# Kernel optimization log

Hardware: AMD Instinct MI355X
Metric: run time of the kernel (lower is better)

The kernel has to match this reference:

```python
import jax, jax.numpy as jnp
import numpy as np

N = 10000      # num nodes
E = 320000     # num edges
IN = 256       # in_dim
MP = 256       # mp_width
FL = 512       # fl_width
OUT = 64       # out_dim


def setup_inputs() -> dict:
    key = jax.random.key(0)
    ks = jax.random.split(key, 20)
    inp = {}
    inp["x"] = jax.random.normal(ks[0], (N, IN), dtype=jnp.float32)
    inp["edge_index"] = jax.random.randint(ks[1], (2, E), 0, N, dtype=jnp.int64)
    # iMP (frozen) linear layers: weight ~ N(0, 1) per nn.init.normal_(std=1.0)
    inp["mp_w0"] = jax.random.normal(ks[2], (IN, MP), dtype=jnp.float32)
    inp["mp_b0"] = jax.random.uniform(ks[3], (MP,), minval=-1.0, maxval=1.0) / np.sqrt(IN)
    inp["mp_w1"] = jax.random.normal(ks[4], (MP, MP), dtype=jnp.float32)
    inp["mp_b1"] = jax.random.uniform(ks[5], (MP,), minval=-1.0, maxval=1.0) / np.sqrt(MP)
    inp["mp_w2"] = jax.random.normal(ks[6], (MP, MP), dtype=jnp.float32)
    inp["mp_b2"] = jax.random.uniform(ks[7], (MP,), minval=-1.0, maxval=1.0) / np.sqrt(MP)
    # FC layers (torch default Linear init scale ~ 1/sqrt(fan_in))
    inp["fc_w0"] = jax.random.normal(ks[8], (MP, FL), dtype=jnp.float32) / np.sqrt(MP)
    inp["fc_b0"] = jnp.zeros((FL,), dtype=jnp.float32)
    inp["fc_w1"] = jax.random.normal(ks[9], (FL, FL), dtype=jnp.float32) / np.sqrt(FL)
    inp["fc_b1"] = jnp.zeros((FL,), dtype=jnp.float32)
    # injection projections
    inp["inj_w0"] = jax.random.normal(ks[10], (MP, FL), dtype=jnp.float32) / np.sqrt(MP)
    inp["inj_b0"] = jnp.zeros((FL,), dtype=jnp.float32)
    inp["inj_w1"] = jax.random.normal(ks[11], (MP, FL), dtype=jnp.float32) / np.sqrt(MP)
    inp["inj_b1"] = jnp.zeros((FL,), dtype=jnp.float32)
    inp["alpha"] = jnp.array(1.0, dtype=jnp.float32)
    inp["out_w"] = jax.random.normal(ks[12], (FL, OUT), dtype=jnp.float32) / np.sqrt(FL)
    inp["out_b"] = jnp.zeros((OUT,), dtype=jnp.float32)
    return inp


def _imp(x, w, b, row, col, deg_inv):
    # h = relu(W x); h /= deg; Ah = scatter_add over row of h[col]
    h = jax.nn.relu(x @ w + b) * deg_inv[:, None]      # [N, out]
    return jnp.zeros_like(h).at[row].add(h[col])       # gather + scatter-add


def reference(x, edge_index, mp_w0, mp_b0, mp_w1, mp_b1, mp_w2, mp_b2,
              fc_w0, fc_b0, fc_w1, fc_b1, inj_w0, inj_b0, inj_w1, inj_b1,
              alpha, out_w, out_b):
    row, col = edge_index[0], edge_index[1]
    deg = jax.ops.segment_sum(jnp.ones((E,), x.dtype), col, num_segments=N)
    # nodes with deg==0 never appear in col so clamping does not change output
    deg_inv = 1.0 / jnp.maximum(deg, 1.0)

    h = _imp(x, mp_w0, mp_b0, row, col, deg_inv)
    h = _imp(h, mp_w1, mp_b1, row, col, deg_inv)
    h = _imp(h, mp_w2, mp_b2, row, col, deg_inv)

    x_inject = h
    h = alpha * (jax.nn.relu(h) @ fc_w0 + fc_b0) + (x_inject @ inj_w0 + inj_b0)
    h = alpha * (jax.nn.relu(h) @ fc_w1 + fc_b1) + (x_inject @ inj_w1 + inj_b1)
    return h @ out_w + out_b
```

## Files before the change

kernel.cpp:

```cpp
#include <hip/hip_runtime.h>

#define N_NODES 10000
#define N_EDGES 320000
#define MPAD 10112
#define NBIN 10048
#define CAP 128
#define ECHUNK 1024
#define EBLKS 313
#define PREP_BLOCKS 1735
#define PREP_TOT 1148480L

typedef unsigned short u16;
typedef short bf16x8 __attribute__((ext_vector_type(8)));
typedef float f32x4 __attribute__((ext_vector_type(4)));

__device__ __forceinline__ u16 f2b(float f) {
  unsigned u = __builtin_bit_cast(unsigned, f);
  unsigned r = u + 0x7fffu + ((u >> 16) & 1u);
  return (u16)(r >> 16);
}
__device__ __forceinline__ unsigned pack2(float a, float b) {
  return (unsigned)f2b(a) | ((unsigned)f2b(b) << 16);
}
__device__ __forceinline__ float blo(unsigned u) { return __builtin_bit_cast(float, u << 16); }
__device__ __forceinline__ float bhi(unsigned u) { return __builtin_bit_cast(float, u & 0xffff0000u); }

struct PP {
  const float *x; const int *ei;
  const float *w0, *w1, *w2, *fcw0, *injw0, *fcw1, *injw1, *outw;
  const float *fcb0, *injb0, *fcb1, *injb1, *alpha, *outb;
  u16 *xb, *w0t, *w1t, *w2t, *wc1t, *wft;
  float *bias1, *bf;
  int *cursor, *deg, *csr;
};

__global__ __launch_bounds__(256) void prep_place(PP P) {
  const int tid = threadIdx.x, bid = blockIdx.x;

  if (bid < EBLKS) {
    const int e0 = bid * ECHUNK;
#pragma unroll
    for (int j = 0; j < ECHUNK; j += 256) {
      int e = e0 + j + tid;
      if (e < N_EDGES) {
        int r = P.ei[e];
        int c = P.ei[N_EDGES + e];
        int pos = atomicAdd(&P.cursor[r], 1);
        if (pos < CAP) P.csr[r * CAP + pos] = c;
        atomicAdd(&P.deg[c], 1);
      }
    }
    return;
  }

  const float alpha = P.alpha[0];
  const long stride = (long)PREP_BLOCKS * 256;
  for (long ii = (long)(bid - EBLKS) * 256 + tid; ii < PREP_TOT; ii += stride) {
    long i = ii;
    if (i < 640000L) {
      float4 v = ((const float4*)P.x)[i];
      uint2 o;
      o.x = pack2(v.x, v.y);
      o.y = pack2(v.z, v.w);
      *(uint2*)(P.xb + 4 * i) = o;
      continue;
    }
    i -= 640000L;
    if (i < 65536) { P.w0t[i] = f2b(P.w0[(i & 255) * 256 + (i >> 8)]); continue; }
    i -= 65536;
    if (i < 65536) { P.w1t[i] = f2b(P.w1[(i & 255) * 256 + (i >> 8)]); continue; }
    i -= 65536;
    if (i < 65536) { P.w2t[i] = f2b(P.w2[(i & 255) * 256 + (i >> 8)]); continue; }
    i -= 65536;
    if (i < 262144) {
      int n = (int)(i >> 9), k = (int)(i & 511);
      float v = (k < 256) ? alpha * P.fcw0[k * 512 + n] : P.injw0[(k - 256) * 512 + n];
      P.wc1t[i] = f2b(v); continue;
    }
    i -= 262144;
    if (i < 49152) {
      int n = (int)(i & 63), k = (int)(i >> 6);
      const float* fr = (k < 512) ? P.fcw1 + (size_t)k * 512
                                  : P.injw1 + (size_t)(k - 512) * 512;
      float a0 = 0.f, a1 = 0.f, a2 = 0.f, a3 = 0.f;
#pragma unroll 4
      for (int j = 0; j < 512; j += 4) {
        float4 f = *(const float4*)(fr + j);
        a0 += f.x * P.outw[(j + 0) * 64 + n];
        a1 += f.y * P.outw[(j + 1) * 64 + n];
        a2 += f.z * P.outw[(j + 2) * 64 + n];
        a3 += f.w * P.outw[(j + 3) * 64 + n];
      }
      float acc = (a0 + a1) + (a2 + a3);
      if (k < 512) acc *= alpha;
      P.wft[n * 768 + k] = f2b(acc);
      continue;
    }
    i -= 49152;
    if (i < 64) {
      float acc = P.outb[i];
#pragma unroll 8
      for (int j = 0; j < 512; ++j)
        acc += (alpha * P.fcb1[j] + P.injb1[j]) * P.outw[j * 64 + i];
      P.bf[i] = acc;
      continue;
    }
    i -= 64;
    if (i < 512) { P.bias1[i] = alpha * P.fcb0[i] + P.injb0[i]; continue; }
  }
}

template<int K, bool RELU, bool SCALE, bool F32OUT>
__global__ __launch_bounds__(128) void gemm64(
    const u16* __restrict__ A, int lda,
    const u16* __restrict__ Bt,
    const float* __restrict__ bias,
    const int* __restrict__ deg,
    u16* __restrict__ Cb, float* __restrict__ Cf, int ldc)
{
  __shared__ u16 As[64 * 72];
  __shared__ u16 Bs[64 * 72];
  const int tid = threadIdx.x;
  const int m0 = blockIdx.x * 64;
  const int n0 = blockIdx.y * 64;
  const int wave = tid >> 6;
  const int lane = tid & 63;
  const int wr = wave * 32;
  const int lm = lane & 15;
  const int koff = (lane >> 4) * 8;

  const int srow = tid >> 2;
  const int scol = (tid & 3) * 16;
  const u16* Ag0 = A + (size_t)(m0 + srow) * lda + scol;
  const u16* Ag1 = A + (size_t)(m0 + srow + 32) * lda + scol;
  const u16* Bg0 = Bt + (size_t)(n0 + srow) * K + scol;
  const u16* Bg1 = Bt + (size_t)(n0 + srow + 32) * K + scol;
  u16* Asw0 = &As[srow * 72 + scol];
  u16* Asw1 = &As[(srow + 32) * 72 + scol];
  u16* Bsw0 = &Bs[srow * 72 + scol];
  u16* Bsw1 = &Bs[(srow + 32) * 72 + scol];

  f32x4 acc[2][4] = {};

  int4 pa0 = *(const int4*)(Ag0),     pa1 = *(const int4*)(Ag0 + 8);
  int4 pa2 = *(const int4*)(Ag1),     pa3 = *(const int4*)(Ag1 + 8);
  int4 pb0 = *(const int4*)(Bg0),     pb1 = *(const int4*)(Bg0 + 8);
  int4 pb2 = *(const int4*)(Bg1),     pb3 = *(const int4*)(Bg1 + 8);

#pragma unroll
  for (int kb = 0; kb < K; kb += 64) {
    __syncthreads();
    *(int4*)Asw0 = pa0; *(int4*)(Asw0 + 8) = pa1;
    *(int4*)Asw1 = pa2; *(int4*)(Asw1 + 8) = pa3;
    *(int4*)Bsw0 = pb0; *(int4*)(Bsw0 + 8) = pb1;
    *(int4*)Bsw1 = pb2; *(int4*)(Bsw1 + 8) = pb3;
    __syncthreads();
    if (kb + 64 < K) {
      pa0 = *(const int4*)(Ag0 + kb + 64); pa1 = *(const int4*)(Ag0 + kb + 72);
      pa2 = *(const int4*)(Ag1 + kb + 64); pa3 = *(const int4*)(Ag1 + kb + 72);
      pb0 = *(const int4*)(Bg0 + kb + 64); pb1 = *(const int4*)(Bg0 + kb + 72);
      pb2 = *(const int4*)(Bg1 + kb + 64); pb3 = *(const int4*)(Bg1 + kb + 72);
    }
#pragma unroll
    for (int ks = 0; ks < 2; ++ks) {
      bf16x8 af[2], bf[4];
#pragma unroll
      for (int mi = 0; mi < 2; ++mi)
        af[mi] = *(const bf16x8*)&As[(wr + mi * 16 + lm) * 72 + ks * 32 + koff];
#pragma unroll
      for (int ni = 0; ni < 4; ++ni)
        bf[ni] = *(const bf16x8*)&Bs[(ni * 16 + lm) * 72 + ks * 32 + koff];
#pragma unroll
      for (int mi = 0; mi < 2; ++mi)
#pragma unroll
        for (int ni = 0; ni < 4; ++ni)
          acc[mi][ni] = __builtin_amdgcn_mfma_f32_16x16x32_bf16(af[mi], bf[ni], acc[mi][ni], 0, 0, 0);
    }
  }

  const int q4 = (lane >> 4) * 4;
#pragma unroll
  for (int mi = 0; mi < 2; ++mi) {
#pragma unroll
    for (int ni = 0; ni < 4; ++ni) {
      const int gc = n0 + ni * 16 + lm;
      const float bv = bias[gc];
#pragma unroll
      for (int r = 0; r < 4; ++r) {
        const int gr = m0 + wr + mi * 16 + q4 + r;
        float v = acc[mi][ni][r] + bv;
        if (RELU) v = fmaxf(v, 0.f);
        if (SCALE) v *= 1.0f / fmaxf((float)deg[gr], 1.0f);
        if (F32OUT) {
          if (gr < N_NODES) Cf[(size_t)gr * ldc + gc] = v;
        } else {
          Cb[(size_t)gr * ldc + gc] = f2b(v);
        }
      }
    }
  }
}

__global__ __launch_bounds__(128) void gemm_fold(
    const u16* __restrict__ Ar,
    const u16* __restrict__ Ah,
    const u16* __restrict__ Bt,
    const float* __restrict__ bias,
    float* __restrict__ Cf)
{
  const int K = 768;
  __shared__ u16 As[64 * 72];
  __shared__ u16 Bs[64 * 72];
  const int tid = threadIdx.x;
  const int m0 = blockIdx.x * 64;
  const int wave = tid >> 6;
  const int lane = tid & 63;
  const int wr = wave * 32;
  const int lm = lane & 15;
  const int koff = (lane >> 4) * 8;

  const int srow = tid >> 2;
  const int scol = (tid & 3) * 16;
  const int ar0 = m0 + srow, ar1 = m0 + srow + 32;
  auto aptr = [&](int row, int col) -> const u16* {
    return (col < 512) ? Ar + (size_t)row * 512 + col
                       : Ah + (size_t)row * 512 + (col - 512);
  };
  const u16* Bg0 = Bt + (size_t)srow * K + scol;
  const u16* Bg1 = Bt + (size_t)(srow + 32) * K + scol;
  u16* Asw0 = &As[srow * 72 + scol];
  u16* Asw1 = &As[(srow + 32) * 72 + scol];
  u16* Bsw0 = &Bs[srow * 72 + scol];
  u16* Bsw1 = &Bs[(srow + 32) * 72 + scol];

  f32x4 acc[2][4] = {};

  int4 pa0 = *(const int4*)aptr(ar0, scol);
  int4 pa1 = *(const int4*)aptr(ar0, scol + 8);
  int4 pa2 = *(const int4*)aptr(ar1, scol);
  int4 pa3 = *(const int4*)aptr(ar1, scol + 8);
  int4 pb0 = *(const int4*)(Bg0), pb1 = *(const int4*)(Bg0 + 8);
  int4 pb2 = *(const int4*)(Bg1), pb3 = *(const int4*)(Bg1 + 8);

#pragma unroll
  for (int kb = 0; kb < K; kb += 64) {
    __syncthreads();
    *(int4*)Asw0 = pa0; *(int4*)(Asw0 + 8) = pa1;
    *(int4*)Asw1 = pa2; *(int4*)(Asw1 + 8) = pa3;
    *(int4*)Bsw0 = pb0; *(int4*)(Bsw0 + 8) = pb1;
    *(int4*)Bsw1 = pb2; *(int4*)(Bsw1 + 8) = pb3;
    __syncthreads();
    if (kb + 64 < K) {
      int c = kb + 64 + scol;
      pa0 = *(const int4*)aptr(ar0, c);
      pa1 = *(const int4*)aptr(ar0, c + 8);
      pa2 = *(const int4*)aptr(ar1, c);
      pa3 = *(const int4*)aptr(ar1, c + 8);
      pb0 = *(const int4*)(Bg0 + kb + 64); pb1 = *(const int4*)(Bg0 + kb + 72);
      pb2 = *(const int4*)(Bg1 + kb + 64); pb3 = *(const int4*)(Bg1 + kb + 72);
    }
#pragma unroll
    for (int ks = 0; ks < 2; ++ks) {
      bf16x8 af[2], bf[4];
#pragma unroll
      for (int mi = 0; mi < 2; ++mi)
        af[mi] = *(const bf16x8*)&As[(wr + mi * 16 + lm) * 72 + ks * 32 + koff];
#pragma unroll
      for (int ni = 0; ni < 4; ++ni)
        bf[ni] = *(const bf16x8*)&Bs[(ni * 16 + lm) * 72 + ks * 32 + koff];
#pragma unroll
      for (int mi = 0; mi < 2; ++mi)
#pragma unroll
        for (int ni = 0; ni < 4; ++ni)
          acc[mi][ni] = __builtin_amdgcn_mfma_f32_16x16x32_bf16(af[mi], bf[ni], acc[mi][ni], 0, 0, 0);
    }
  }

  const int q4 = (lane >> 4) * 4;
#pragma unroll
  for (int mi = 0; mi < 2; ++mi) {
#pragma unroll
    for (int ni = 0; ni < 4; ++ni) {
      const int gc = ni * 16 + lm;
      const float bv = bias[gc];
#pragma unroll
      for (int r = 0; r < 4; ++r) {
        const int gr = m0 + wr + mi * 16 + q4 + r;
        if (gr < N_NODES) Cf[(size_t)gr * 64 + gc] = acc[mi][ni][r] + bv;
      }
    }
  }
}

__global__ __launch_bounds__(256) void aggregate(
    const u16* __restrict__ tmp, const int* __restrict__ cnt,
    const int* __restrict__ csr, u16* __restrict__ out0,
    u16* __restrict__ A1, int mode)
{
  const int wv = threadIdx.x >> 6;
  const int lane = threadIdx.x & 63;
  const int r = blockIdx.x * 4 + wv;
  const int half = lane >> 5;
  const int q = lane & 31;
  int n = cnt[r]; if (n > CAP) n = CAP;
  const int beg = r * CAP, end = beg + n;
  const size_t feat = (size_t)q * 16;
  const char* tb = (const char*)tmp;

  float s0 = 0.f, s1 = 0.f, s2 = 0.f, s3 = 0.f, s4 = 0.f, s5 = 0.f, s6 = 0.f, s7 = 0.f;
  int i = beg;
  for (; i + 8 <= end; i += 8) {
    uint4 v[4];
#pragma unroll
    for (int j = 0; j < 4; ++j)
      v[j] = *(const uint4*)(tb + (size_t)csr[i + 2 * j + half] * 512 + feat);
#pragma unroll
    for (int j = 0; j < 4; ++j) {
      s0 += blo(v[j].x); s1 += bhi(v[j].x); s2 += blo(v[j].y); s3 += bhi(v[j].y);
      s4 += blo(v[j].z); s5 += bhi(v[j].z); s6 += blo(v[j].w); s7 += bhi(v[j].w);
    }
  }
  for (; i < end; i += 2) {
    int id = i + half;
    if (id < end) {
      uint4 v = *(const uint4*)(tb + (size_t)csr[id] * 512 + feat);
      s0 += blo(v.x); s1 += bhi(v.x); s2 += blo(v.y); s3 += bhi(v.y);
      s4 += blo(v.z); s5 += bhi(v.z); s6 += blo(v.w); s7 += bhi(v.w);
    }
  }
  const int src = lane ^ 32;
  s0 += __shfl(s0, src, 64); s1 += __shfl(s1, src, 64);
  s2 += __shfl(s2, src, 64); s3 += __shfl(s3, src, 64);
  s4 += __shfl(s4, src, 64); s5 += __shfl(s5, src, 64);
  s6 += __shfl(s6, src, 64); s7 += __shfl(s7, src, 64);

  if (half == 0) {
    uint4 pv;
    pv.x = pack2(s0, s1); pv.y = pack2(s2, s3);
    pv.z = pack2(s4, s5); pv.w = pack2(s6, s7);
    if (mode == 0) {
      *(uint4*)((char*)out0 + (size_t)r * 512 + feat) = pv;
    } else {
      uint4 pr;
      pr.x = pack2(fmaxf(s0, 0.f), fmaxf(s1, 0.f));
      pr.y = pack2(fmaxf(s2, 0.f), fmaxf(s3, 0.f));
      pr.z = pack2(fmaxf(s4, 0.f), fmaxf(s5, 0.f));
      pr.w = pack2(fmaxf(s6, 0.f), fmaxf(s7, 0.f));
      *(uint4*)((char*)A1 + (size_t)r * 1024 + feat) = pr;
      *(uint4*)((char*)A1 + (size_t)r * 1024 + 512 + feat) = pv;
    }
  }
}

extern "C" void kernel_launch(void* const* d_in, const int* in_sizes, int n_in,
                              void* d_out, int out_size, void* d_ws, size_t ws_size,
                              hipStream_t stream) {
  const int* ei = (const int*)d_in[1];

  char* p = (char*)d_ws;
  auto carve = [&](size_t bytes) -> void* {
    void* r = (void*)p;
    p += (bytes + 255) & ~(size_t)255;
    return r;
  };
  int*   deg     = (int*)carve(MPAD * 4);
  int*   cursor  = (int*)carve(NBIN * 4);
  int*   csr     = (int*)carve((size_t)NBIN * CAP * 4);
  float* bias1   = (float*)carve(512 * 4);
  float* bf      = (float*)carve(64 * 4);
  u16* xb    = (u16*)carve((size_t)MPAD * 256 * 2);
  u16* w0t   = (u16*)carve(65536 * 2);
  u16* w1t   = (u16*)carve(65536 * 2);
  u16* w2t   = (u16*)carve(65536 * 2);
  u16* wc1t  = (u16*)carve(262144 * 2);
  u16* wft   = (u16*)carve(49152 * 2);
  u16* tmp   = (u16*)carve((size_t)MPAD * 256 * 2);
  u16* h     = (u16*)carve((size_t)MPAD * 256 * 2);
  u16* cat1  = (u16*)carve((size_t)MPAD * 512 * 2);
  u16* relu1 = (u16*)carve((size_t)MPAD * 512 * 2);

  PP pp;
  pp.x = (const float*)d_in[0];
  pp.ei = ei;
  pp.w0 = (const float*)d_in[2];
  pp.w1 = (const float*)d_in[4];
  pp.w2 = (const float*)d_in[6];
  pp.fcw0 = (const float*)d_in[8];
  pp.fcw1 = (const float*)d_in[10];
  pp.injw0 = (const float*)d_in[12];
  pp.injw1 = (const float*)d_in[14];
  pp.outw = (const float*)d_in[17];
  pp.fcb0 = (const float*)d_in[9];
  pp.injb0 = (const float*)d_in[13];
  pp.fcb1 = (const float*)d_in[11];
  pp.injb1 = (const float*)d_in[15];
  pp.alpha = (const float*)d_in[16];
  pp.outb = (const float*)d_in[18];
  pp.xb = xb; pp.w0t = w0t; pp.w1t = w1t; pp.w2t = w2t;
  pp.wc1t = wc1t; pp.wft = wft;
  pp.bias1 = bias1; pp.bf = bf;
  pp.cursor = cursor; pp.deg = deg; pp.csr = csr;

  const float* mp_b0 = (const float*)d_in[3];
  const float* mp_b1 = (const float*)d_in[5];
  const float* mp_b2 = (const float*)d_in[7];
  float* out = (float*)d_out;

  hipMemsetAsync(deg, 0, (size_t)(MPAD + NBIN) * 4, stream);
  prep_place<<<EBLKS + PREP_BLOCKS, 256, 0, stream>>>(pp);

  dim3 gmp(MPAD / 64, 4), gfc(MPAD / 64, 8), go(MPAD / 64, 1);
  gemm64<256, true, true, false><<<gmp, 128, 0, stream>>>(xb, 256, w0t, mp_b0, deg, tmp, nullptr, 256);
  aggregate<<<2500, 256, 0, stream>>>(tmp, cursor, csr, h, nullptr, 0);
  gemm64<256, true, true, false><<<gmp, 128, 0, stream>>>(h, 256, w1t, mp_b1, deg, tmp, nullptr, 256);
  aggregate<<<2500, 256, 0, stream>>>(tmp, cursor, csr, h, nullptr, 0);
  gemm64<256, true, true, false><<<gmp, 128, 0, stream>>>(h, 256, w2t, mp_b2, deg, tmp, nullptr, 256);
  aggregate<<<2500, 256, 0, stream>>>(tmp, cursor, csr, nullptr, cat1, 1);
  gemm64<512, true, false, false><<<gfc, 128, 0, stream>>>(cat1, 512, wc1t, bias1, nullptr, relu1, nullptr, 512);
  gemm_fold<<<go, 128, 0, stream>>>(relu1, cat1 + 256, wft, bf, out);
}
```

Before: 241.1 us.

## Fuse CSR edge placement with first MP GEMM and move degree scaling into aggregation

Edge placement (CSR build and degree counting) now runs in the same launch as the first message-passing GEMM instead of sharing a launch with weight conversion. This is possible because the 1/deg scaling moves out of the GEMM epilogue and into the gather in aggregate, where each neighbor's value is scaled by its reciprocal degree. The CSR column indices are stored as 16-bit values to halve index traffic, and the prep kernel gets fewer blocks. The cost is an extra degree lookup and rcp per gathered edge, plus approximate reciprocal precision.

Result: no change. 237.8 us (-1.4%).

```diff
diff --git a/kernel.cpp b/kernel.cpp
--- a/kernel.cpp
+++ b/kernel.cpp
@@ -7,7 +7,8 @@
 #define CAP 128
 #define ECHUNK 1024
 #define EBLKS 313
-#define PREP_BLOCKS 1735
+#define GT1 632
+#define PREP_BLOCKS 1024
 #define PREP_TOT 1148480L
 
 typedef unsigned short u16;
@@ -26,36 +27,17 @@
 __device__ __forceinline__ float bhi(unsigned u) { return __builtin_bit_cast(float, u & 0xffff0000u); }
 
 struct PP {
-  const float *x; const int *ei;
+  const float *x;
   const float *w0, *w1, *w2, *fcw0, *injw0, *fcw1, *injw1, *outw;
   const float *fcb0, *injb0, *fcb1, *injb1, *alpha, *outb;
   u16 *xb, *w0t, *w1t, *w2t, *wc1t, *wft;
   float *bias1, *bf;
-  int *cursor, *deg, *csr;
 };
 
-__global__ __launch_bounds__(256) void prep_place(PP P) {
-  const int tid = threadIdx.x, bid = blockIdx.x;
-
-  if (bid < EBLKS) {
-    const int e0 = bid * ECHUNK;
-#pragma unroll
-    for (int j = 0; j < ECHUNK; j += 256) {
-      int e = e0 + j + tid;
-      if (e < N_EDGES) {
-        int r = P.ei[e];
-        int c = P.ei[N_EDGES + e];
-        int pos = atomicAdd(&P.cursor[r], 1);
-        if (pos < CAP) P.csr[r * CAP + pos] = c;
-        atomicAdd(&P.deg[c], 1);
-      }
-    }
-    return;
-  }
-
+__global__ __launch_bounds__(256) void prep(PP P) {
   const float alpha = P.alpha[0];
   const long stride = (long)PREP_BLOCKS * 256;
-  for (long ii = (long)(bid - EBLKS) * 256 + tid; ii < PREP_TOT; ii += stride) {
+  for (long ii = (long)blockIdx.x * 256 + threadIdx.x; ii < PREP_TOT; ii += stride) {
     long i = ii;
     if (i < 640000L) {
       float4 v = ((const float4*)P.x)[i];
@@ -110,19 +92,15 @@
   }
 }
 
-template<int K, bool RELU, bool SCALE, bool F32OUT>
-__global__ __launch_bounds__(128) void gemm64(
+template<int K, bool RELU, bool F32OUT>
+__device__ __forceinline__ void gemm_tile(
+    int m0, int n0,
     const u16* __restrict__ A, int lda,
     const u16* __restrict__ Bt,
     const float* __restrict__ bias,
-    const int* __restrict__ deg,
-    u16* __restrict__ Cb, float* __restrict__ Cf, int ldc)
+    u16* __restrict__ Cb, float* __restrict__ Cf, int ldc,
+    u16* As, u16* Bs, int tid)
 {
-  __shared__ u16 As[64 * 72];
-  __shared__ u16 Bs[64 * 72];
-  const int tid = threadIdx.x;
-  const int m0 = blockIdx.x * 64;
-  const int n0 = blockIdx.y * 64;
   const int wave = tid >> 6;
   const int lane = tid & 63;
   const int wr = wave * 32;
@@ -190,7 +168,6 @@
         const int gr = m0 + wr + mi * 16 + q4 + r;
         float v = acc[mi][ni][r] + bv;
         if (RELU) v = fmaxf(v, 0.f);
-        if (SCALE) v *= 1.0f / fmaxf((float)deg[gr], 1.0f);
         if (F32OUT) {
           if (gr < N_NODES) Cf[(size_t)gr * ldc + gc] = v;
         } else {
@@ -199,6 +176,49 @@
       }
     }
   }
+}
+
+template<int K, bool RELU, bool F32OUT>
+__global__ __launch_bounds__(128) void gemm64(
+    const u16* __restrict__ A, int lda,
+    const u16* __restrict__ Bt,
+    const float* __restrict__ bias,
+    u16* __restrict__ Cb, float* __restrict__ Cf, int ldc)
+{
+  __shared__ u16 As[64 * 72];
+  __shared__ u16 Bs[64 * 72];
+  gemm_tile<K, RELU, F32OUT>(blockIdx.x * 64, blockIdx.y * 64,
+                             A, lda, Bt, bias, Cb, Cf, ldc, As, Bs, threadIdx.x);
+}
+
+__global__ __launch_bounds__(128) void place_gemm1(
+    const int* __restrict__ ei, int* __restrict__ cursor, int* __restrict__ deg,
+    u16* __restrict__ csr,
+    const u16* __restrict__ xb, const u16* __restrict__ w0t,
+    const float* __restrict__ mp_b0, u16* __restrict__ tmp)
+{
+  __shared__ u16 As[64 * 72];
+  __shared__ u16 Bs[64 * 72];
+  const int bid = blockIdx.x, tid = threadIdx.x;
+
+  if (bid < EBLKS) {
+    const int e0 = bid * ECHUNK;
+#pragma unroll
+    for (int j = 0; j < ECHUNK; j += 128) {
+      int e = e0 + j + tid;
+      if (e < N_EDGES) {
+        int r = ei[e];
+        int c = ei[N_EDGES + e];
+        int pos = atomicAdd(&cursor[r], 1);
+        if (pos < CAP) csr[r * CAP + pos] = (u16)c;
+        atomicAdd(&deg[c], 1);
+      }
+    }
+    return;
+  }
+  const int t = bid - EBLKS;
+  gemm_tile<256, true, false>((t % 158) * 64, (t / 158) * 64,
+                              xb, 256, w0t, mp_b0, tmp, nullptr, 256, As, Bs, tid);
 }
 
 __global__ __launch_bounds__(128) void gemm_fold(
@@ -294,8 +314,8 @@
 
 __global__ __launch_bounds__(256) void aggregate(
     const u16* __restrict__ tmp, const int* __restrict__ cnt,
-    const int* __restrict__ csr, u16* __restrict__ out0,
-    u16* __restrict__ A1, int mode)
+    const u16* __restrict__ csr, const int* __restrict__ deg,
+    u16* __restrict__ out0, u16* __restrict__ A1, int mode)
 {
   const int wv = threadIdx.x >> 6;
   const int lane = threadIdx.x & 63;
@@ -310,22 +330,32 @@
   float s0 = 0.f, s1 = 0.f, s2 = 0.f, s3 = 0.f, s4 = 0.f, s5 = 0.f, s6 = 0.f, s7 = 0.f;
   int i = beg;
   for (; i + 8 <= end; i += 8) {
-    uint4 v[4];
+    int c[4]; uint4 v[4]; float sc[4];
+#pragma unroll
+    for (int j = 0; j < 4; ++j) c[j] = csr[i + 2 * j + half];
+#pragma unroll
+    for (int j = 0; j < 4; ++j) v[j] = *(const uint4*)(tb + (size_t)c[j] * 512 + feat);
 #pragma unroll
     for (int j = 0; j < 4; ++j)
-      v[j] = *(const uint4*)(tb + (size_t)csr[i + 2 * j + half] * 512 + feat);
+      sc[j] = __builtin_amdgcn_rcpf(fmaxf((float)deg[c[j]], 1.0f));
 #pragma unroll
     for (int j = 0; j < 4; ++j) {
-      s0 += blo(v[j].x); s1 += bhi(v[j].x); s2 += blo(v[j].y); s3 += bhi(v[j].y);
-      s4 += blo(v[j].z); s5 += bhi(v[j].z); s6 += blo(v[j].w); s7 += bhi(v[j].w);
+      s0 += blo(v[j].x) * sc[j]; s1 += bhi(v[j].x) * sc[j];
+      s2 += blo(v[j].y) * sc[j]; s3 += bhi(v[j].y) * sc[j];
+      s4 += blo(v[j].z) * sc[j]; s5 += bhi(v[j].z) * sc[j];
+      s6 += blo(v[j].w) * sc[j]; s7 += bhi(v[j].w) * sc[j];
     }
   }
   for (; i < end; i += 2) {
     int id = i + half;
     if (id < end) {
-      uint4 v = *(const uint4*)(tb + (size_t)csr[id] * 512 + feat);
-      s0 += blo(v.x); s1 += bhi(v.x); s2 += blo(v.y); s3 += bhi(v.y);
-      s4 += blo(v.z); s5 += bhi(v.z); s6 += blo(v.w); s7 += bhi(v.w);
+      int c = csr[id];
+      uint4 v = *(const uint4*)(tb + (size_t)c * 512 + feat);
+      float sc = __builtin_amdgcn_rcpf(fmaxf((float)deg[c], 1.0f));
+      s0 += blo(v.x) * sc; s1 += bhi(v.x) * sc;
+      s2 += blo(v.y) * sc; s3 += bhi(v.y) * sc;
+      s4 += blo(v.z) * sc; s5 += bhi(v.z) * sc;
+      s6 += blo(v.w) * sc; s7 += bhi(v.w) * sc;
     }
   }
   const int src = lane ^ 32;
@@ -365,7 +395,7 @@
   };
   int*   deg     = (int*)carve(MPAD * 4);
   int*   cursor  = (int*)carve(NBIN * 4);
-  int*   csr     = (int*)carve((size_t)NBIN * CAP * 4);
+  u16*   csr     = (u16*)carve((size_t)NBIN * CAP * 2);
   float* bias1   = (float*)carve(512 * 4);
   float* bf      = (float*)carve(64 * 4);
   u16* xb    = (u16*)carve((size_t)MPAD * 256 * 2);
@@ -381,7 +411,6 @@
 
   PP pp;
   pp.x = (const float*)d_in[0];
-  pp.ei = ei;
   pp.w0 = (const float*)d_in[2];
   pp.w1 = (const float*)d_in[4];
   pp.w2 = (const float*)d_in[6];
@@ -399,7 +428,6 @@
   pp.xb = xb; pp.w0t = w0t; pp.w1t = w1t; pp.w2t = w2t;
   pp.wc1t = wc1t; pp.wft = wft;
   pp.bias1 = bias1; pp.bf = bf;
-  pp.cursor = cursor; pp.deg = deg; pp.csr = csr;
 
   const float* mp_b0 = (const float*)d_in[3];
   const float* mp_b1 = (const float*)d_in[5];
@@ -407,15 +435,16 @@
   float* out = (float*)d_out;
 
   hipMemsetAsync(deg, 0, (size_t)(MPAD + NBIN) * 4, stream);
-  prep_place<<<EBLKS + PREP_BLOCKS, 256, 0, stream>>>(pp);
+  prep<<<PREP_BLOCKS, 256, 0, stream>>>(pp);
+  place_gemm1<<<EBLKS + GT1, 128, 0, stream>>>(ei, cursor, deg, csr,
+                                               xb, w0t, mp_b0, tmp);
 
   dim3 gmp(MPAD / 64, 4), gfc(MPAD / 64, 8), go(MPAD / 64, 1);
-  gemm64<256, true, true, false><<<gmp, 128, 0, stream>>>(xb, 256, w0t, mp_b0, deg, tmp, nullptr, 256);
-  aggregate<<<2500, 256, 0, stream>>>(tmp, cursor, csr, h, nullptr, 0);
-  gemm64<256, true, true, false><<<gmp, 128, 0, stream>>>(h, 256, w1t, mp_b1, deg, tmp, nullptr, 256);
-  aggregate<<<2500, 256, 0, stream>>>(tmp, cursor, csr, h, nullptr, 0);
-  gemm64<256, true, true, false><<<gmp, 128, 0, stream>>>(h, 256, w2t, mp_b2, deg, tmp, nullptr, 256);
-  aggregate<<<2500, 256, 0, stream>>>(tmp, cursor, csr, nullptr, cat1, 1);
-  gemm64<512, true, false, false><<<gfc, 128, 0, stream>>>(cat1, 512, wc1t, bias1, nullptr, relu1, nullptr, 512);
+  aggregate<<<2500, 256, 0, stream>>>(tmp, cursor, csr, deg, h, nullptr, 0);
+  gemm64<256, true, false><<<gmp, 128, 0, stream>>>(h, 256, w1t, mp_b1, tmp, nullptr, 256);
+  aggregate<<<2500, 256, 0, stream>>>(tmp, cursor, csr, deg, h, nullptr, 0);
+  gemm64<256, true, false><<<gmp, 128, 0, stream>>>(h, 256, w2t, mp_b2, tmp, nullptr, 256);
+  aggregate<<<2500, 256, 0, stream>>>(tmp, cursor, csr, deg, nullptr, cat1, 1);
+  gemm64<512, true, false><<<gfc, 128, 0, stream>>>(cat1, 512, wc1t, bias1, relu1, nullptr, 512);
   gemm_fold<<<go, 128, 0, stream>>>(relu1, cat1 + 256, wft, bf, out);
 }
```
